# Optimization experiments

Hardware: AMD Instinct MI355X
Metric: run time of the kernel (lower is better)

Reference implementation:

```python
import jax, jax.numpy as jnp
import numpy as np

EPS = 1e-5
elu = jax.nn.elu

def bn(x, g, b):
    # BatchNorm (training-mode stats), channel axis = 1
    axes = tuple(i for i in range(x.ndim) if i != 1)
    m = x.mean(axes, keepdims=True)
    v = x.var(axes, keepdims=True)
    shp = [1] * x.ndim; shp[1] = -1
    return g.reshape(shp) * (x - m) * jax.lax.rsqrt(v + EPS) + b.reshape(shp)

def setup_inputs() -> dict:
    key = jax.random.key(0)
    B, N, M, K, C, H, O = 8, 8192, 2048, 16, 128, 64, 256
    ks = jax.random.split(key, 16)
    d = {}
    d['q_points'] = jax.random.normal(ks[0], (B, 3, M), jnp.float32)
    d['s_points'] = jax.random.normal(ks[1], (B, 3, N), jnp.float32)
    d['s_feats'] = jax.random.normal(ks[2], (B, C, N), jnp.float32)
    d['f1_w'] = jax.random.normal(ks[3], (H, 3), jnp.float32) * 0.1
    d['f1_b'] = jnp.zeros((H,), jnp.float32); d['f1_g'] = jnp.ones((H,), jnp.float32); d['f1_be'] = jnp.zeros((H,), jnp.float32)
    d['f2_w'] = jax.random.normal(ks[4], (H, H), jnp.float32) * 0.1
    d['f2_b'] = jnp.zeros((H,), jnp.float32); d['f2_g'] = jnp.ones((H,), jnp.float32); d['f2_be'] = jnp.zeros((H,), jnp.float32)
    d['stem_w'] = jax.random.normal(ks[5], (K * K, 3, K), jnp.float32) * 0.1
    d['stem_b'] = jnp.zeros((K * K,), jnp.float32); d['stem_g'] = jnp.ones((K * K,), jnp.float32); d['stem_be'] = jnp.zeros((K * K,), jnp.float32)
    d['x1_w'] = jax.random.normal(ks[6], (K, K, K), jnp.float32) * 0.1
    d['x1_b'] = jnp.zeros((K * K,), jnp.float32); d['x1_g'] = jnp.ones((K * K,), jnp.float32); d['x1_be'] = jnp.zeros((K * K,), jnp.float32)
    d['x2_w'] = jax.random.normal(ks[7], (K, K, K), jnp.float32) * 0.1
    d['x2_b'] = jnp.zeros((K * K,), jnp.float32); d['x2_g'] = jnp.ones((K * K,), jnp.float32); d['x2_be'] = jnp.zeros((K * K,), jnp.float32)
    d['dw_w'] = jax.random.normal(ks[8], (C + H, K), jnp.float32) * 0.1
    d['pw_w'] = jax.random.normal(ks[9], (O, C + H), jnp.float32) * 0.1
    d['pw_b'] = jnp.zeros((O,), jnp.float32); d['sep_g'] = jnp.ones((O,), jnp.float32); d['sep_be'] = jnp.zeros((O,), jnp.float32)
    d['neighbor_indices'] = jax.random.randint(ks[10], (B, M, K), 0, N, jnp.int64)
    return d

def reference(q_points, s_points, s_feats, f1_w, f1_b, f1_g, f1_be,
              f2_w, f2_b, f2_g, f2_be, stem_w, stem_b, stem_g, stem_be,
              x1_w, x1_b, x1_g, x1_be, x2_w, x2_b, x2_g, x2_be,
              dw_w, pw_w, pw_b, sep_g, sep_be, neighbor_indices):
    B, _, M = q_points.shape
    K = neighbor_indices.shape[2]
    bidx = jnp.arange(B)[:, None, None]
    # group_gather: [B,3,M,K] neighbor coords, centered on queries
    sp = jnp.swapaxes(s_points, 1, 2)                      # [B,N,3]
    aligned = jnp.transpose(sp[bidx, neighbor_indices], (0, 3, 1, 2)) - q_points[:, :, :, None]
    sf = jnp.swapaxes(s_feats, 1, 2)                       # [B,N,C]
    nbr = jnp.transpose(sf[bidx, neighbor_indices], (0, 3, 1, 2))  # [B,C,M,K]
    # f_shared_mlp: two 1x1 conv blocks (conv -> ELU -> BN)
    h = bn(elu(jnp.einsum('bcmk,oc->bomk', aligned, f1_w) + f1_b[None, :, None, None]), f1_g, f1_be)
    h = bn(elu(jnp.einsum('bcmk,oc->bomk', h, f2_w) + f2_b[None, :, None, None]), f2_g, f2_be)
    nf = jnp.concatenate([nbr, h], axis=1)                 # [B,C+H,M,K]
    # X-transform shared MLP: stem Conv2d(3 -> K*K, (1,K))
    t = jnp.einsum('bcmk,ock->bom', aligned, stem_w) + stem_b[None, :, None]
    t = bn(elu(t), stem_g, stem_be).reshape(B, K, K, M)    # [B,g,j,M]
    for w, bb, g, be in ((x1_w, x1_b, x1_g, x1_be), (x2_w, x2_b, x2_g, x2_be)):
        # grouped Conv2d(K -> K*K, (K,1), groups=K)
        y = jnp.einsum('bgjm,gpj->bgpm', t, w) + bb.reshape(1, K, K, 1)
        y = bn(elu(y.reshape(B, K * K, M)), g, be).reshape(B, K, K, M)
        t = jnp.swapaxes(y, 1, 2)                          # XReshape transpose(1,2)
    x = jnp.transpose(t, (0, 3, 2, 1))                     # [B,M,K,K]
    # batched matmul: feats^T @ X
    qf = jnp.einsum('bcmk,bmkl->bcml', nf, x)              # [B,C+H,M,K]
    # SeparableConv2d (1,K): depthwise over K then pointwise 1x1, ELU, BN
    dw = jnp.einsum('bcmk,ck->bcm', qf, dw_w)
    out = jnp.einsum('bcm,oc->bom', dw, pw_w) + pw_b[None, :, None]
    out = bn(elu(out), sep_g, sep_be)                      # [B,O,M]
    return out
```

## Files before the change

### kernel.cpp

```cpp
#include <hip/hip_runtime.h>
#include <hip/hip_bf16.h>
#include <cstddef>
#include <cstdint>

constexpr int cB = 8, cN = 8192, cM = 2048, cK = 16, cC = 128, cH = 64, cO = 256, cCH = 192;
constexpr int NPTS = cB * cM;
constexpr float cEPS = 1e-5f;

typedef __attribute__((ext_vector_type(8))) short short8;
typedef __attribute__((ext_vector_type(4))) float f32x4;

constexpr size_t ACC_BN1 = 0, ACC_BN2 = 128, ACC_STEM = 256, ACC_X1 = 768, ACC_X2 = 1280, ACC_FIN = 1792;
constexpr size_t OFF_SFT = 8192;
constexpr size_t OFF_H2  = OFF_SFT + (size_t)cB * cN * 64;
constexpr size_t OFF_TST = OFF_H2 + (size_t)NPTS * 512;
constexpr size_t OFF_Y1  = OFF_TST + (size_t)NPTS * 128;
constexpr size_t OFF_Y2  = OFF_Y1 + (size_t)NPTS * 256;
constexpr size_t OFF_AL  = OFF_Y2 + (size_t)NPTS * 128;
constexpr size_t OFF_DW  = OFF_Y1;
constexpr size_t WS_FLOATS = OFF_Y2 + (size_t)NPTS * 256;

__device__ __forceinline__ float eluf(float x) { return x > 0.f ? x : __expf(x) - 1.f; }

__device__ __forceinline__ uint32_t pk2bf(float a, float b) {
    uint32_t ua = __float_as_uint(a); ua += 0x7FFFu + ((ua >> 16) & 1u);
    uint32_t ub = __float_as_uint(b); ub += 0x7FFFu + ((ub >> 16) & 1u);
    return (ua >> 16) | (ub & 0xFFFF0000u);
}
__device__ __forceinline__ float bf_lo(uint32_t u) { return __uint_as_float(u << 16); }
__device__ __forceinline__ float bf_hi(uint32_t u) { return __uint_as_float(u & 0xFFFF0000u); }
__device__ __forceinline__ uint16_t f2bf_u(float a) {
    uint32_t ua = __float_as_uint(a); ua += 0x7FFFu + ((ua >> 16) & 1u);
    return (uint16_t)(ua >> 16);
}

#define WAVE_SYNC() do { asm volatile("s_waitcnt lgkmcnt(0)" ::: "memory"); \
                         __builtin_amdgcn_sched_barrier(0); } while (0)

__global__ __launch_bounds__(256) void k_tr(const float* __restrict__ sf, float* __restrict__ ws) {
    __shared__ float tA[32][33];
    __shared__ float tBt[32][33];
    int b = blockIdx.z, n0 = blockIdx.x * 32, c0 = blockIdx.y * 32;
    int tx = threadIdx.x, ty = threadIdx.y;
    #pragma unroll
    for (int j = 0; j < 32; j += 8) {
        tA[ty + j][tx]  = sf[((size_t)b * cC + (c0 + ty + j)) * cN + n0 + tx];
        tBt[ty + j][tx] = sf[((size_t)b * cC + 64 + (c0 + ty + j)) * cN + n0 + tx];
    }
    __syncthreads();
    uint32_t* out = (uint32_t*)(ws + OFF_SFT);
    #pragma unroll
    for (int j = 0; j < 32; j += 8)
        out[((size_t)b * cN + (n0 + ty + j)) * 64 + c0 + tx] = pk2bf(tA[tx][ty + j], tBt[tx][ty + j]);
}

__global__ __launch_bounds__(256) void kA(const float* __restrict__ qp, const float* __restrict__ sp,
        const float* __restrict__ f1w, const float* __restrict__ f1b,
        const float* __restrict__ stw, const float* __restrict__ stb,
        const int* __restrict__ nidx, float* __restrict__ ws) {
    __shared__ float alw[4][4][48];
    __shared__ __align__(16) uint16_t albs[16][64];
    __shared__ __align__(16) uint16_t tstt[16][256];
    __shared__ float red[640];
    int t = threadIdx.x, lane = t & 63, w = t >> 6;
    int ncol = lane & 15, g = lane >> 4;
    for (int l = t; l < 640; l += 256) red[l] = 0.f;
    __syncthreads();
    short8 bfr[4][2];
    float sbias[4];
    #pragma unroll
    for (int tt = 0; tt < 4; tt++) {
        int o = w*64 + tt*16 + ncol;
        sbias[tt] = stb[o];
        #pragma unroll
        for (int s = 0; s < 2; s++) {
            short8 bb;
            #pragma unroll
            for (int j = 0; j < 8; j++) {
                int Kk = s*32 + g*8 + j;
                bb[j] = (Kk < 48) ? (short)f2bf_u(stw[(size_t)o*48 + Kk]) : (short)0;
            }
            bfr[tt][s] = bb;
        }
    }
    float w0 = f1w[lane*3], w1 = f1w[lane*3+1], w2 = f1w[lane*3+2], fb = f1b[lane];
    int pt0 = blockIdx.x * 16;
    {
        int p = lane >> 4, k = lane & 15;
        int row = w*4 + p;
        int pt = pt0 + row, b = pt >> 11, m = pt & (cM - 1);
        int id = nidx[(size_t)pt * cK + k];
        #pragma unroll
        for (int c = 0; c < 3; c++) {
            float v = sp[((size_t)b*3 + c)*cN + id] - qp[((size_t)b*3 + c)*cM + m];
            alw[w][p][c*16 + k] = v;
            int bo = ((c*16 + k)*2) ^ ((row & 7) << 4);
            *(uint16_t*)((char*)&albs[row][0] + bo) = f2bf_u(v);
        }
        int bo = ((48 + k)*2) ^ ((row & 7) << 4);
        *(uint16_t*)((char*)&albs[row][0] + bo) = 0;
    }
    WAVE_SYNC();
    {
        float* alg = ws + OFF_AL;
        const float* srcA = &alw[w][0][0];
        int ptw = pt0 + w*4;
        #pragma unroll
        for (int i = 0; i < 3; i++)
            alg[(size_t)ptw*48 + i*64 + lane] = srcA[i*64 + lane];
    }
    float ps1 = 0, pss1 = 0;
    #pragma unroll
    for (int p = 0; p < 4; p++) {
        #pragma unroll
        for (int k = 0; k < 16; k++) {
            float a0 = alw[w][p][k], a1 = alw[w][p][16 + k], a2 = alw[w][p][32 + k];
            float e = eluf(fb + w0*a0 + w1*a1 + w2*a2);
            ps1 += e; pss1 += e*e;
        }
    }
    atomicAdd(&red[512 + lane], ps1); atomicAdd(&red[576 + lane], pss1);
    __syncthreads();
    short8 a0, a1;
    {
        int b0 = (g*16) ^ ((ncol & 7) << 4);
        int b1 = (64 + g*16) ^ ((ncol & 7) << 4);
        a0 = *(const short8*)((const char*)&albs[ncol][0] + b0);
        a1 = *(const short8*)((const char*)&albs[ncol][0] + b1);
    }
    #pragma unroll
    for (int tt = 0; tt < 4; tt++) {
        f32x4 acc = {0.f, 0.f, 0.f, 0.f};
        acc = __builtin_amdgcn_mfma_f32_16x16x32_bf16(a0, bfr[tt][0], acc, 0, 0, 0);
        acc = __builtin_amdgcn_mfma_f32_16x16x32_bf16(a1, bfr[tt][1], acc, 0, 0, 0);
        int o = w*64 + tt*16 + ncol;
        float ps2 = 0, pss2 = 0;
        #pragma unroll
        for (int r = 0; r < 4; r++) {
            float e = eluf(acc[r] + sbias[tt]);
            ps2 += e; pss2 += e*e;
            tstt[g*4 + r][o] = f2bf_u(e);
        }
        atomicAdd(&red[o], ps2); atomicAdd(&red[256 + o], pss2);
    }
    __syncthreads();
    {
        uint4* tst4 = (uint4*)(ws + OFF_TST);
        const uint4* srcT = (const uint4*)&tstt[0][0];
        tst4[(size_t)pt0*32 + t]       = srcT[t];
        tst4[(size_t)pt0*32 + 256 + t] = srcT[256 + t];
    }
    atomicAdd(&ws[ACC_STEM + t], red[t]);
    atomicAdd(&ws[ACC_STEM + 256 + t], red[256 + t]);
    if (t < 64) { atomicAdd(&ws[ACC_BN1 + t], red[512 + t]); atomicAdd(&ws[ACC_BN1 + 64 + t], red[576 + t]); }
}

__global__ __launch_bounds__(256) void kC(const float* __restrict__ f1w, const float* __restrict__ f1b,
        const float* __restrict__ f2w, const float* __restrict__ f2b,
        const float* __restrict__ f1g, const float* __restrict__ f1be, float* __restrict__ ws) {
    __shared__ float alw[4][4][48];
    __shared__ __align__(16) unsigned char h1l[4][4][2048];
    __shared__ float s1s[64], sh1s[64], b2s[64];
    __shared__ float red[128];
    int t = threadIdx.x, lane = t & 63, w = t >> 6;
    if (t < 128) red[t] = 0.f;
    if (t < 64) {
        float mn = ws[ACC_BN1 + t] * (1.f/262144.f);
        float vr = ws[ACC_BN1 + 64 + t] * (1.f/262144.f) - mn*mn;
        float s = f1g[t] * rsqrtf(vr + cEPS);
        s1s[t] = s; sh1s[t] = f1be[t] - mn*s;
    }
    __syncthreads();
    float w0 = f1w[lane*3], w1 = f1w[lane*3+1], w2 = f1w[lane*3+2], fb = f1b[lane];
    int ncol = lane & 15, g = lane >> 4;
    if (t < 64) {
        float a = f2b[t];
        const float* fr = f2w + (size_t)t*64;
        #pragma unroll 8
        for (int c = 0; c < 64; c++) a += fr[c] * sh1s[c];
        b2s[t] = a;
    }
    short8 bfr[4][2];
    #pragma unroll
    for (int tt = 0; tt < 4; tt++) {
        int o = tt*16 + ncol;
        #pragma unroll
        for (int s = 0; s < 2; s++) {
            short8 bb;
            #pragma unroll
            for (int j = 0; j < 8; j++) {
                int c = s*32 + g*8 + j;
                bb[j] = (short)f2bf_u(f2w[(size_t)o*64 + c] * s1s[c]);
            }
            bfr[tt][s] = bb;
        }
    }
    __syncthreads();
    float bias2[4];
    #pragma unroll
    for (int tt = 0; tt < 4; tt++) bias2[tt] = b2s[tt*16 + ncol];
    int ptw = blockIdx.x * 16 + w * 4;
    {
        const float* alg = ws + OFF_AL;
        float* dst = &alw[w][0][0];
        #pragma unroll
        for (int i = 0; i < 3; i++)
            dst[i*64 + lane] = alg[(size_t)ptw*48 + i*64 + lane];
    }
    WAVE_SYNC();
    #pragma unroll
    for (int p = 0; p < 4; p++) {
        #pragma unroll
        for (int k = 0; k < 16; k++) {
            float a0 = alw[w][p][k], a1 = alw[w][p][16 + k], a2 = alw[w][p][32 + k];
            float e = eluf(fb + w0*a0 + w1*a1 + w2*a2);
            int byteoff = (lane*2) ^ ((k & 7) << 4);
            *(uint16_t*)&h1l[w][p][k*128 + byteoff] = (uint16_t)f2bf_u(e);
        }
    }
    WAVE_SYNC();
    float ps[4] = {0,0,0,0}, pss[4] = {0,0,0,0};
    int b0o = (g*16) ^ ((ncol & 7) << 4);
    int b1o = (64 + g*16) ^ ((ncol & 7) << 4);
    short8 a0v[4], a1v[4];
    #pragma unroll
    for (int p = 0; p < 4; p++) {
        a0v[p] = *(const short8*)&h1l[w][p][ncol*128 + b0o];
        a1v[p] = *(const short8*)&h1l[w][p][ncol*128 + b1o];
    }
    WAVE_SYNC();
    #pragma unroll
    for (int p = 0; p < 4; p++) {
        #pragma unroll
        for (int tt = 0; tt < 4; tt++) {
            f32x4 acc = {0.f, 0.f, 0.f, 0.f};
            acc = __builtin_amdgcn_mfma_f32_16x16x32_bf16(a0v[p], bfr[tt][0], acc, 0, 0, 0);
            acc = __builtin_amdgcn_mfma_f32_16x16x32_bf16(a1v[p], bfr[tt][1], acc, 0, 0, 0);
            float e0 = eluf(acc[0] + bias2[tt]);
            float e1 = eluf(acc[1] + bias2[tt]);
            float e2 = eluf(acc[2] + bias2[tt]);
            float e3 = eluf(acc[3] + bias2[tt]);
            ps[tt]  += e0+e1+e2+e3;
            pss[tt] += e0*e0+e1*e1+e2*e2+e3*e3;
            int o = tt*16 + ncol;
            *(uint2*)&h1l[w][p][o*32 + g*8] = make_uint2(pk2bf(e0, e1), pk2bf(e2, e3));
        }
    }
    WAVE_SYNC();
    {
        uint4* dst = (uint4*)((uint32_t*)(ws + OFF_H2) + (size_t)ptw*512);
        const uint4* srcH = (const uint4*)&h1l[w][0][0];
        #pragma unroll
        for (int i = 0; i < 8; i++)
            dst[i*64 + lane] = srcH[i*64 + lane];
    }
    #pragma unroll
    for (int tt = 0; tt < 4; tt++) {
        int o = tt*16 + ncol;
        atomicAdd(&red[o], ps[tt]); atomicAdd(&red[64 + o], pss[tt]);
    }
    __syncthreads();
    if (t < 64) { atomicAdd(&ws[ACC_BN2 + t], red[t]); atomicAdd(&ws[ACC_BN2 + 64 + t], red[64 + t]); }
}

__global__ __launch_bounds__(256) void kE(const float* __restrict__ x1w, const float* __restrict__ x1b,
        const float* __restrict__ stg, const float* __restrict__ stbe, float* __restrict__ ws) {
    __shared__ float xw[256 * 17];
    __shared__ float ts[4][4][256];
    __shared__ float red[512];
    int t = threadIdx.x, lane = t & 63, w = t >> 6;
    for (int l = t; l < 4096; l += 256) xw[(l >> 4)*17 + (l & 15)] = x1w[l];
    for (int l = t; l < 512; l += 256) red[l] = 0.f;
    float sscl[4], sshf[4];
    #pragma unroll
    for (int i = 0; i < 4; i++) {
        int ch = lane*4 + i;
        float mn = ws[ACC_STEM + ch] * (1.f/16384.f);
        float vr = ws[ACC_STEM + 256 + ch] * (1.f/16384.f) - mn*mn;
        float s = stg[ch] * rsqrtf(vr + cEPS);
        sscl[i] = s; sshf[i] = stbe[ch] - mn*s;
    }
    __syncthreads();
    const uint16_t* tstb = (const uint16_t*)(ws + OFF_TST);
    int pt0 = blockIdx.x * 16 + w * 4;
    #pragma unroll
    for (int p = 0; p < 4; p++) {
        uint2 v2 = *(const uint2*)&tstb[(size_t)(pt0 + p)*256 + lane*4];
        ts[w][p][lane*4+0] = sscl[0]*bf_lo(v2.x) + sshf[0];
        ts[w][p][lane*4+1] = sscl[1]*bf_hi(v2.x) + sshf[1];
        ts[w][p][lane*4+2] = sscl[2]*bf_lo(v2.y) + sshf[2];
        ts[w][p][lane*4+3] = sscl[3]*bf_hi(v2.y) + sshf[3];
    }
    WAVE_SYNC();
    float eo[4][4];
    #pragma unroll
    for (int sl = 0; sl < 4; sl++) {
        int o = (sl < 2) ? (lane*2 + sl) : (128 + lane*2 + sl - 2);
        int gg = o >> 4;
        float bia = x1b[o];
        float a0 = bia, a1 = bia, a2 = bia, a3 = bia;
        #pragma unroll
        for (int j4 = 0; j4 < 4; j4++) {
            float s0 = xw[o*17 + j4*4], s1 = xw[o*17 + j4*4+1], s2 = xw[o*17 + j4*4+2], s3 = xw[o*17 + j4*4+3];
            float4 t0 = *(const float4*)&ts[w][0][gg*16 + j4*4];
            float4 t1 = *(const float4*)&ts[w][1][gg*16 + j4*4];
            float4 t2 = *(const float4*)&ts[w][2][gg*16 + j4*4];
            float4 t3 = *(const float4*)&ts[w][3][gg*16 + j4*4];
            a0 += s0*t0.x + s1*t0.y + s2*t0.z + s3*t0.w;
            a1 += s0*t1.x + s1*t1.y + s2*t1.z + s3*t1.w;
            a2 += s0*t2.x + s1*t2.y + s2*t2.z + s3*t2.w;
            a3 += s0*t3.x + s1*t3.y + s2*t3.z + s3*t3.w;
        }
        eo[0][sl] = eluf(a0); eo[1][sl] = eluf(a1); eo[2][sl] = eluf(a2); eo[3][sl] = eluf(a3);
        float ps = eo[0][sl]+eo[1][sl]+eo[2][sl]+eo[3][sl];
        float qs = eo[0][sl]*eo[0][sl]+eo[1][sl]*eo[1][sl]+eo[2][sl]*eo[2][sl]+eo[3][sl]*eo[3][sl];
        atomicAdd(&red[o], ps); atomicAdd(&red[256 + o], qs);
    }
    uint32_t* y1p = (uint32_t*)(ws + OFF_Y1);
    #pragma unroll
    for (int p = 0; p < 4; p++) {
        y1p[(size_t)(pt0 + p)*128 + lane]      = pk2bf(eo[p][0], eo[p][1]);
        y1p[(size_t)(pt0 + p)*128 + 64 + lane] = pk2bf(eo[p][2], eo[p][3]);
    }
    __syncthreads();
    atomicAdd(&ws[ACC_X1 + t], red[t]); atomicAdd(&ws[ACC_X1 + 256 + t], red[256 + t]);
}

__global__ __launch_bounds__(256) void kG(const float* __restrict__ x2w, const float* __restrict__ x2b,
        const float* __restrict__ x1g, const float* __restrict__ x1be, float* __restrict__ ws) {
    __shared__ float xw[256 * 17];
    __shared__ float ts[4][4][256];
    __shared__ float red[512];
    int t = threadIdx.x, lane = t & 63, w = t >> 6;
    for (int l = t; l < 4096; l += 256) xw[(l >> 4)*17 + (l & 15)] = x2w[l];
    for (int l = t; l < 512; l += 256) red[l] = 0.f;
    float sscl[4], sshf[4];
    #pragma unroll
    for (int i = 0; i < 4; i++) {
        int ch = lane*4 + i;
        float mn = ws[ACC_X1 + ch] * (1.f/16384.f);
        float vr = ws[ACC_X1 + 256 + ch] * (1.f/16384.f) - mn*mn;
        float s = x1g[ch] * rsqrtf(vr + cEPS);
        sscl[i] = s; sshf[i] = x1be[ch] - mn*s;
    }
    __syncthreads();
    const uint32_t* y1p = (const uint32_t*)(ws + OFF_Y1);
    int pt0 = blockIdx.x * 16 + w * 4;
    #pragma unroll
    for (int p = 0; p < 4; p++) {
        uint2 v2 = *(const uint2*)(y1p + (size_t)(pt0 + p)*128 + lane*2);
        float vv[4] = { sscl[0]*bf_lo(v2.x) + sshf[0], sscl[1]*bf_hi(v2.x) + sshf[1],
                        sscl[2]*bf_lo(v2.y) + sshf[2], sscl[3]*bf_hi(v2.y) + sshf[3] };
        #pragma unroll
        for (int i = 0; i < 4; i++) {
            int ch = lane*4 + i;
            ts[w][p][((ch & 15) << 4) | (ch >> 4)] = vv[i];
        }
    }
    WAVE_SYNC();
    float eo[4][4];
    #pragma unroll
    for (int sl = 0; sl < 4; sl++) {
        int o = (sl < 2) ? (lane*2 + sl) : (128 + lane*2 + sl - 2);
        int gg = o >> 4;
        float bia = x2b[o];
        float a0 = bia, a1 = bia, a2 = bia, a3 = bia;
        #pragma unroll
        for (int j4 = 0; j4 < 4; j4++) {
            float s0 = xw[o*17 + j4*4], s1 = xw[o*17 + j4*4+1], s2 = xw[o*17 + j4*4+2], s3 = xw[o*17 + j4*4+3];
            float4 t0 = *(const float4*)&ts[w][0][gg*16 + j4*4];
            float4 t1 = *(const float4*)&ts[w][1][gg*16 + j4*4];
            float4 t2 = *(const float4*)&ts[w][2][gg*16 + j4*4];
            float4 t3 = *(const float4*)&ts[w][3][gg*16 + j4*4];
            a0 += s0*t0.x + s1*t0.y + s2*t0.z + s3*t0.w;
            a1 += s0*t1.x + s1*t1.y + s2*t1.z + s3*t1.w;
            a2 += s0*t2.x + s1*t2.y + s2*t2.z + s3*t2.w;
            a3 += s0*t3.x + s1*t3.y + s2*t3.z + s3*t3.w;
        }
        eo[0][sl] = eluf(a0); eo[1][sl] = eluf(a1); eo[2][sl] = eluf(a2); eo[3][sl] = eluf(a3);
        float ps = eo[0][sl]+eo[1][sl]+eo[2][sl]+eo[3][sl];
        float qs = eo[0][sl]*eo[0][sl]+eo[1][sl]*eo[1][sl]+eo[2][sl]*eo[2][sl]+eo[3][sl]*eo[3][sl];
        atomicAdd(&red[o], ps); atomicAdd(&red[256 + o], qs);
    }
    uint32_t* y2p = (uint32_t*)(ws + OFF_Y2);
    #pragma unroll
    for (int p = 0; p < 4; p++) {
        y2p[(size_t)(pt0 + p)*128 + lane]      = pk2bf(eo[p][0], eo[p][1]);
        y2p[(size_t)(pt0 + p)*128 + 64 + lane] = pk2bf(eo[p][2], eo[p][3]);
    }
    __syncthreads();
    atomicAdd(&ws[ACC_X2 + t], red[t]); atomicAdd(&ws[ACC_X2 + 256 + t], red[256 + t]);
}

__global__ __launch_bounds__(256) void kI(const float* __restrict__ dww,
        const float* __restrict__ f2g, const float* __restrict__ f2be,
        const float* __restrict__ x2g, const float* __restrict__ x2be,
        const int* __restrict__ nidx, float* __restrict__ ws) {
    __shared__ float dws[192 * 17];
    __shared__ float xs[4][256];
    const uint32_t* h2p = (const uint32_t*)(ws + OFF_H2);
    const uint32_t* sfp = (const uint32_t*)(ws + OFF_SFT);
    const uint32_t* y2p = (const uint32_t*)(ws + OFF_Y2);
    int t = threadIdx.x, lane = t & 63, w = t >> 6;
    for (int l = t; l < 3072; l += 256) dws[(l >> 4)*17 + (l & 15)] = dww[l];
    float sx[4], shx[4];
    #pragma unroll
    for (int i = 0; i < 4; i++) {
        int ch = lane*4 + i;
        float mn = ws[ACC_X2 + ch] * (1.f/16384.f);
        float vr = ws[ACC_X2 + 256 + ch] * (1.f/16384.f) - mn*mn;
        float s = x2g[ch] * rsqrtf(vr + cEPS);
        sx[i] = s; shx[i] = x2be[ch] - mn*s;
    }
    float s2, sh2;
    {
        float mn = ws[ACC_BN2 + lane] * (1.f/262144.f);
        float vr = ws[ACC_BN2 + 64 + lane] * (1.f/262144.f) - mn*mn;
        s2 = f2g[lane] * rsqrtf(vr + cEPS);
        sh2 = f2be[lane] - mn*s2;
    }
    __syncthreads();
    uint16_t* dwb = (uint16_t*)(ws + OFF_DW);
    int pt0 = blockIdx.x * 8 + w * 2;
    for (int p = 0; p < 2; p++) {
        int pt = pt0 + p, b = pt >> 11;
        const int4* ip = (const int4*)(nidx + (size_t)pt * cK);
        int4 iA = ip[0], iB = ip[1], iC2 = ip[2], iD = ip[3];
        int idxv[16] = {iA.x, iA.y, iA.z, iA.w, iB.x, iB.y, iB.z, iB.w,
                        iC2.x, iC2.y, iC2.z, iC2.w, iD.x, iD.y, iD.z, iD.w};
        float nfa[16], nfb[16];
        #pragma unroll
        for (int k = 0; k < 16; k++) {
            uint32_t u = sfp[((size_t)b*cN + idxv[k]) * 64 + lane];
            nfa[k] = bf_lo(u); nfb[k] = bf_hi(u);
        }
        float nfh[16];
        {
            const uint4* srcq = (const uint4*)(h2p + (size_t)pt*512 + lane*8);
            uint4 ha = srcq[0], hbq = srcq[1];
            nfh[0]  = s2*bf_lo(ha.x)  + sh2; nfh[1]  = s2*bf_hi(ha.x)  + sh2;
            nfh[2]  = s2*bf_lo(ha.y)  + sh2; nfh[3]  = s2*bf_hi(ha.y)  + sh2;
            nfh[4]  = s2*bf_lo(ha.z)  + sh2; nfh[5]  = s2*bf_hi(ha.z)  + sh2;
            nfh[6]  = s2*bf_lo(ha.w)  + sh2; nfh[7]  = s2*bf_hi(ha.w)  + sh2;
            nfh[8]  = s2*bf_lo(hbq.x) + sh2; nfh[9]  = s2*bf_hi(hbq.x) + sh2;
            nfh[10] = s2*bf_lo(hbq.y) + sh2; nfh[11] = s2*bf_hi(hbq.y) + sh2;
            nfh[12] = s2*bf_lo(hbq.z) + sh2; nfh[13] = s2*bf_hi(hbq.z) + sh2;
            nfh[14] = s2*bf_lo(hbq.w) + sh2; nfh[15] = s2*bf_hi(hbq.w) + sh2;
        }
        {
            uint2 v2 = *(const uint2*)(y2p + (size_t)pt*128 + lane*2);
            xs[w][lane*4+0] = sx[0]*bf_lo(v2.x) + shx[0];
            xs[w][lane*4+1] = sx[1]*bf_hi(v2.x) + shx[1];
            xs[w][lane*4+2] = sx[2]*bf_lo(v2.y) + shx[2];
            xs[w][lane*4+3] = sx[3]*bf_hi(v2.y) + shx[3];
        }
        WAVE_SYNC();
        float qc[16];
        #pragma unroll
        for (int l = 0; l < 16; l++) qc[l] = 0.f;
        #pragma unroll
        for (int k = 0; k < 16; k++) {
            float4 x0 = *(const float4*)&xs[w][k*16 + 0];
            float4 x1 = *(const float4*)&xs[w][k*16 + 4];
            float4 x2v = *(const float4*)&xs[w][k*16 + 8];
            float4 x3 = *(const float4*)&xs[w][k*16 + 12];
            float nh = nfh[k];
            qc[0] += nh*x0.x; qc[1] += nh*x0.y; qc[2]  += nh*x0.z; qc[3]  += nh*x0.w;
            qc[4] += nh*x1.x; qc[5] += nh*x1.y; qc[6]  += nh*x1.z; qc[7]  += nh*x1.w;
            qc[8] += nh*x2v.x; qc[9] += nh*x2v.y; qc[10] += nh*x2v.z; qc[11] += nh*x2v.w;
            qc[12] += nh*x3.x; qc[13] += nh*x3.y; qc[14] += nh*x3.z; qc[15] += nh*x3.w;
        }
        float dc = 0;
        #pragma unroll
        for (int l = 0; l < 16; l++) dc += qc[l] * dws[(lane + 128)*17 + l];
        float qa[16], qb[16];
        #pragma unroll
        for (int l = 0; l < 16; l++) { qa[l] = 0.f; qb[l] = 0.f; }
        #pragma unroll
        for (int k = 0; k < 16; k++) {
            float4 x0 = *(const float4*)&xs[w][k*16 + 0];
            float4 x1 = *(const float4*)&xs[w][k*16 + 4];
            float4 x2v = *(const float4*)&xs[w][k*16 + 8];
            float4 x3 = *(const float4*)&xs[w][k*16 + 12];
            float na = nfa[k], nb = nfb[k];
            qa[0] += na*x0.x; qa[1] += na*x0.y; qa[2]  += na*x0.z; qa[3]  += na*x0.w;
            qa[4] += na*x1.x; qa[5] += na*x1.y; qa[6]  += na*x1.z; qa[7]  += na*x1.w;
            qa[8] += na*x2v.x; qa[9] += na*x2v.y; qa[10] += na*x2v.z; qa[11] += na*x2v.w;
            qa[12] += na*x3.x; qa[13] += na*x3.y; qa[14] += na*x3.z; qa[15] += na*x3.w;
            qb[0] += nb*x0.x; qb[1] += nb*x0.y; qb[2]  += nb*x0.z; qb[3]  += nb*x0.w;
            qb[4] += nb*x1.x; qb[5] += nb*x1.y; qb[6]  += nb*x1.z; qb[7]  += nb*x1.w;
            qb[8] += nb*x2v.x; qb[9] += nb*x2v.y; qb[10] += nb*x2v.z; qb[11] += nb*x2v.w;
            qb[12] += nb*x3.x; qb[13] += nb*x3.y; qb[14] += nb*x3.z; qb[15] += nb*x3.w;
        }
        float da = 0, db = 0;
        #pragma unroll
        for (int l = 0; l < 16; l++) {
            da += qa[l] * dws[lane*17 + l];
            db += qb[l] * dws[(lane + 64)*17 + l];
        }
        uint16_t* op = dwb + (size_t)pt * cCH;
        op[lane] = f2bf_u(da); op[lane + 64] = f2bf_u(db); op[lane + 128] = f2bf_u(dc);
        WAVE_SYNC();
    }
}

__global__ __launch_bounds__(256) void kJ(const float* __restrict__ pww, const float* __restrict__ pwb,
                                          float* __restrict__ ws, float* __restrict__ out) {
    __shared__ float red[128];
    int t = threadIdx.x, lane = t & 63, w = t >> 6;
    int ncol = lane & 15, g = lane >> 4;
    if (t < 128) red[t] = 0.f;
    __syncthreads();
    int p0 = blockIdx.x * 64;
    int otile = blockIdx.y * 64 + w * 16;
    short8 afr[6];
    #pragma unroll
    for (int kt = 0; kt < 6; kt++) {
        const float* src = pww + (size_t)(otile + ncol) * cCH + kt*32 + g*8;
        float4 v0 = *(const float4*)src;
        float4 v1 = *(const float4*)(src + 4);
        short8 aa;
        aa[0] = (short)f2bf_u(v0.x); aa[1] = (short)f2bf_u(v0.y);
        aa[2] = (short)f2bf_u(v0.z); aa[3] = (short)f2bf_u(v0.w);
        aa[4] = (short)f2bf_u(v1.x); aa[5] = (short)f2bf_u(v1.y);
        aa[6] = (short)f2bf_u(v1.z); aa[7] = (short)f2bf_u(v1.w);
        afr[kt] = aa;
    }
    float pb[4];
    #pragma unroll
    for (int r = 0; r < 4; r++) pb[r] = pwb[otile + g*4 + r];
    const uint16_t* dwb = (const uint16_t*)(ws + OFF_DW);
    int bb = p0 >> 11, mb0 = p0 & (cM - 1);
    float psum[4] = {0,0,0,0}, pssq[4] = {0,0,0,0};
    #pragma unroll
    for (int mt = 0; mt < 4; mt++) {
        const uint16_t* brow = dwb + (size_t)(p0 + mt*16 + ncol) * cCH;
        f32x4 acc = {0.f, 0.f, 0.f, 0.f};
        #pragma unroll
        for (int kt = 0; kt < 6; kt++) {
            short8 bfr = *(const short8*)&brow[kt*32 + g*8];
            acc = __builtin_amdgcn_mfma_f32_16x16x32_bf16(afr[kt], bfr, acc, 0, 0, 0);
        }
        #pragma unroll
        for (int r = 0; r < 4; r++) {
            float e = eluf(acc[r] + pb[r]);
            psum[r] += e; pssq[r] += e*e;
            out[((size_t)bb*cO + otile + g*4 + r)*cM + mb0 + mt*16 + ncol] = e;
        }
    }
    #pragma unroll
    for (int r = 0; r < 4; r++) {
        float s_ = psum[r], q_ = pssq[r];
        #pragma unroll
        for (int off = 1; off < 16; off <<= 1) { s_ += __shfl_xor(s_, off); q_ += __shfl_xor(q_, off); }
        if (ncol == 0) {
            atomicAdd(&red[w*16 + g*4 + r], s_);
            atomicAdd(&red[64 + w*16 + g*4 + r], q_);
        }
    }
    __syncthreads();
    if (t < 64) {
        atomicAdd(&ws[ACC_FIN + blockIdx.y*64 + t], red[t]);
        atomicAdd(&ws[ACC_FIN + 256 + blockIdx.y*64 + t], red[64 + t]);
    }
}

__global__ __launch_bounds__(256) void kK(float* __restrict__ out, const float* __restrict__ ws,
        const float* __restrict__ sepg, const float* __restrict__ sepbe) {
    int i = blockIdx.x * 256 + threadIdx.x;
    if (i < (cB*cO*cM) / 4) {
        int o = (i >> 9) & 255;
        float mn = ws[ACC_FIN + o] * (1.f/16384.f);
        float vr = ws[ACC_FIN + 256 + o] * (1.f/16384.f) - mn*mn;
        float s = sepg[o] * rsqrtf(vr + cEPS);
        float sh = sepbe[o] - mn*s;
        float4 v = ((float4*)out)[i];
        v.x = s*v.x + sh; v.y = s*v.y + sh; v.z = s*v.z + sh; v.w = s*v.w + sh;
        ((float4*)out)[i] = v;
    }
}

extern "C" void kernel_launch(void* const* d_in, const int* in_sizes, int n_in,
                              void* d_out, int out_size, void* d_ws, size_t ws_size,
                              hipStream_t stream) {
    const float* qp   = (const float*)d_in[0];
    const float* sp   = (const float*)d_in[1];
    const float* sf   = (const float*)d_in[2];
    const float* f1w  = (const float*)d_in[3];
    const float* f1b  = (const float*)d_in[4];
    const float* f1g  = (const float*)d_in[5];
    const float* f1be = (const float*)d_in[6];
    const float* f2w  = (const float*)d_in[7];
    const float* f2b  = (const float*)d_in[8];
    const float* f2g  = (const float*)d_in[9];
    const float* f2be = (const float*)d_in[10];
    const float* stw  = (const float*)d_in[11];
    const float* stb  = (const float*)d_in[12];
    const float* stg  = (const float*)d_in[13];
    const float* stbe = (const float*)d_in[14];
    const float* x1w  = (const float*)d_in[15];
    const float* x1b  = (const float*)d_in[16];
    const float* x1g  = (const float*)d_in[17];
    const float* x1be = (const float*)d_in[18];
    const float* x2w  = (const float*)d_in[19];
    const float* x2b  = (const float*)d_in[20];
    const float* x2g  = (const float*)d_in[21];
    const float* x2be = (const float*)d_in[22];
    const float* dww  = (const float*)d_in[23];
    const float* pww  = (const float*)d_in[24];
    const float* pwb  = (const float*)d_in[25];
    const float* sepg = (const float*)d_in[26];
    const float* sepbe= (const float*)d_in[27];
    const int*   nidx = (const int*)d_in[28];
    float* ws  = (float*)d_ws;
    float* out = (float*)d_out;
    if (ws_size < WS_FLOATS * sizeof(float)) return;

    hipMemsetAsync(d_ws, 0, 2304 * sizeof(float), stream);
    k_tr<<<dim3(cN/32, 2, cB), dim3(32, 8), 0, stream>>>(sf, ws);
    kA<<<NPTS/16, 256, 0, stream>>>(qp, sp, f1w, f1b, stw, stb, nidx, ws);
    kC<<<NPTS/16, 256, 0, stream>>>(f1w, f1b, f2w, f2b, f1g, f1be, ws);
    kE<<<NPTS/16, 256, 0, stream>>>(x1w, x1b, stg, stbe, ws);
    kG<<<NPTS/16, 256, 0, stream>>>(x2w, x2b, x1g, x1be, ws);
    kI<<<NPTS/8,  256, 0, stream>>>(dww, f2g, f2be, x2g, x2be, nidx, ws);
    kJ<<<dim3(NPTS/64, cO/64), 256, 0, stream>>>(pww, pwb, ws, out);
    kK<<<(cB*cO*cM/4 + 255)/256, 256, 0, stream>>>(out, ws, sepg, sepbe);
}
```

Before: 244.6 us.

## Merge independent kernels into block-partitioned launches to overlap transpose and stages

Folds the feature transpose into kA as extra blocks, and runs kC and kE together in one launch, picking the branch from the block index. The stages merged in each pair have no data dependency on each other, so they can run concurrently, filling the GPU better and saving launch gaps. kC also now writes h2 straight to global memory instead of staging it through LDS. The cost is that the merged kernels get the union of shared-memory footprints (about 37 KB for kCE), which can lower occupancy for the lighter branch.

```diff
diff --git a/kernel.cpp b/kernel.cpp
--- a/kernel.cpp
+++ b/kernel.cpp
@@ -37,32 +37,36 @@
 #define WAVE_SYNC() do { asm volatile("s_waitcnt lgkmcnt(0)" ::: "memory"); \
                          __builtin_amdgcn_sched_barrier(0); } while (0)
 
-__global__ __launch_bounds__(256) void k_tr(const float* __restrict__ sf, float* __restrict__ ws) {
-    __shared__ float tA[32][33];
-    __shared__ float tBt[32][33];
-    int b = blockIdx.z, n0 = blockIdx.x * 32, c0 = blockIdx.y * 32;
-    int tx = threadIdx.x, ty = threadIdx.y;
-    #pragma unroll
-    for (int j = 0; j < 32; j += 8) {
-        tA[ty + j][tx]  = sf[((size_t)b * cC + (c0 + ty + j)) * cN + n0 + tx];
-        tBt[ty + j][tx] = sf[((size_t)b * cC + 64 + (c0 + ty + j)) * cN + n0 + tx];
-    }
-    __syncthreads();
-    uint32_t* out = (uint32_t*)(ws + OFF_SFT);
-    #pragma unroll
-    for (int j = 0; j < 32; j += 8)
-        out[((size_t)b * cN + (n0 + ty + j)) * 64 + c0 + tx] = pk2bf(tA[tx][ty + j], tBt[tx][ty + j]);
-}
-
-__global__ __launch_bounds__(256) void kA(const float* __restrict__ qp, const float* __restrict__ sp,
+__global__ __launch_bounds__(256) void kAT(const float* __restrict__ qp, const float* __restrict__ sp,
         const float* __restrict__ f1w, const float* __restrict__ f1b,
         const float* __restrict__ stw, const float* __restrict__ stb,
-        const int* __restrict__ nidx, float* __restrict__ ws) {
-    __shared__ float alw[4][4][48];
-    __shared__ __align__(16) uint16_t albs[16][64];
-    __shared__ __align__(16) uint16_t tstt[16][256];
-    __shared__ float red[640];
-    int t = threadIdx.x, lane = t & 63, w = t >> 6;
+        const float* __restrict__ sf, const int* __restrict__ nidx, float* __restrict__ ws) {
+    __shared__ __align__(16) unsigned char smem[15872];
+    int t = threadIdx.x;
+    if (blockIdx.x >= 1024) {
+        float* tA = (float*)smem;
+        float* tB = (float*)(smem + 4224);
+        int id = blockIdx.x - 1024;
+        int n0 = (id & 255) * 32, c0 = ((id >> 8) & 1) * 32, b = id >> 9;
+        int tx = t & 31, ty = t >> 5;
+        #pragma unroll
+        for (int j = 0; j < 32; j += 8) {
+            tA[(ty + j)*33 + tx] = sf[((size_t)b * cC + (c0 + ty + j)) * cN + n0 + tx];
+            tB[(ty + j)*33 + tx] = sf[((size_t)b * cC + 64 + (c0 + ty + j)) * cN + n0 + tx];
+        }
+        __syncthreads();
+        uint32_t* outp = (uint32_t*)(ws + OFF_SFT);
+        #pragma unroll
+        for (int j = 0; j < 32; j += 8)
+            outp[((size_t)b * cN + (n0 + ty + j)) * 64 + c0 + tx] =
+                pk2bf(tA[tx*33 + ty + j], tB[tx*33 + ty + j]);
+        return;
+    }
+    float (*alw)[4][48]   = (float(*)[4][48])smem;
+    uint16_t (*albs)[64]  = (uint16_t(*)[64])(smem + 3072);
+    uint16_t (*tstt)[256] = (uint16_t(*)[256])(smem + 5120);
+    float* red            = (float*)(smem + 13312);
+    int lane = t & 63, w = t >> 6;
     int ncol = lane & 15, g = lane >> 4;
     for (int l = t; l < 640; l += 256) red[l] = 0.f;
     __syncthreads();
@@ -155,175 +159,175 @@
     if (t < 64) { atomicAdd(&ws[ACC_BN1 + t], red[512 + t]); atomicAdd(&ws[ACC_BN1 + 64 + t], red[576 + t]); }
 }
 
-__global__ __launch_bounds__(256) void kC(const float* __restrict__ f1w, const float* __restrict__ f1b,
+__global__ __launch_bounds__(256) void kCE(const float* __restrict__ f1w, const float* __restrict__ f1b,
         const float* __restrict__ f2w, const float* __restrict__ f2b,
-        const float* __restrict__ f1g, const float* __restrict__ f1be, float* __restrict__ ws) {
-    __shared__ float alw[4][4][48];
-    __shared__ __align__(16) unsigned char h1l[4][4][2048];
-    __shared__ float s1s[64], sh1s[64], b2s[64];
-    __shared__ float red[128];
+        const float* __restrict__ f1g, const float* __restrict__ f1be,
+        const float* __restrict__ x1w, const float* __restrict__ x1b,
+        const float* __restrict__ stg, const float* __restrict__ stbe, float* __restrict__ ws) {
+    __shared__ __align__(16) unsigned char smem[37120];
     int t = threadIdx.x, lane = t & 63, w = t >> 6;
-    if (t < 128) red[t] = 0.f;
-    if (t < 64) {
-        float mn = ws[ACC_BN1 + t] * (1.f/262144.f);
-        float vr = ws[ACC_BN1 + 64 + t] * (1.f/262144.f) - mn*mn;
-        float s = f1g[t] * rsqrtf(vr + cEPS);
-        s1s[t] = s; sh1s[t] = f1be[t] - mn*s;
-    }
-    __syncthreads();
-    float w0 = f1w[lane*3], w1 = f1w[lane*3+1], w2 = f1w[lane*3+2], fb = f1b[lane];
-    int ncol = lane & 15, g = lane >> 4;
-    if (t < 64) {
-        float a = f2b[t];
-        const float* fr = f2w + (size_t)t*64;
-        #pragma unroll 8
-        for (int c = 0; c < 64; c++) a += fr[c] * sh1s[c];
-        b2s[t] = a;
-    }
-    short8 bfr[4][2];
-    #pragma unroll
-    for (int tt = 0; tt < 4; tt++) {
-        int o = tt*16 + ncol;
-        #pragma unroll
-        for (int s = 0; s < 2; s++) {
-            short8 bb;
+    if (blockIdx.x < 1024) {
+        float (*alw)[4][48] = (float(*)[4][48])smem;
+        unsigned char (*h1l)[4][2048] = (unsigned char(*)[4][2048])(smem + 3072);
+        float* s1s  = (float*)(smem + 35840);
+        float* sh1s = (float*)(smem + 36096);
+        float* b2s  = (float*)(smem + 36352);
+        float* red  = (float*)(smem + 36608);
+        if (t < 128) red[t] = 0.f;
+        if (t < 64) {
+            float mn = ws[ACC_BN1 + t] * (1.f/262144.f);
+            float vr = ws[ACC_BN1 + 64 + t] * (1.f/262144.f) - mn*mn;
+            float s = f1g[t] * rsqrtf(vr + cEPS);
+            s1s[t] = s; sh1s[t] = f1be[t] - mn*s;
+        }
+        __syncthreads();
+        float w0 = f1w[lane*3], w1 = f1w[lane*3+1], w2 = f1w[lane*3+2], fb = f1b[lane];
+        int ncol = lane & 15, g = lane >> 4;
+        if (t < 64) {
+            float a = f2b[t];
+            const float* fr = f2w + (size_t)t*64;
+            #pragma unroll 8
+            for (int c = 0; c < 64; c++) a += fr[c] * sh1s[c];
+            b2s[t] = a;
+        }
+        short8 bfr[4][2];
+        #pragma unroll
+        for (int tt = 0; tt < 4; tt++) {
+            int o = tt*16 + ncol;
             #pragma unroll
-            for (int j = 0; j < 8; j++) {
-                int c = s*32 + g*8 + j;
-                bb[j] = (short)f2bf_u(f2w[(size_t)o*64 + c] * s1s[c]);
+            for (int s = 0; s < 2; s++) {
+                short8 bb;
+                #pragma unroll
+                for (int j = 0; j < 8; j++) {
+                    int c = s*32 + g*8 + j;
+                    bb[j] = (short)f2bf_u(f2w[(size_t)o*64 + c] * s1s[c]);
+                }
+                bfr[tt][s] = bb;
             }
-            bfr[tt][s] = bb;
-        }
-    }
-    __syncthreads();
-    float bias2[4];
-    #pragma unroll
-    for (int tt = 0; tt < 4; tt++) bias2[tt] = b2s[tt*16 + ncol];
-    int ptw = blockIdx.x * 16 + w * 4;
+        }
+        __syncthreads();
+        float bias2[4];
+        #pragma unroll
+        for (int tt = 0; tt < 4; tt++) bias2[tt] = b2s[tt*16 + ncol];
+        int ptw = blockIdx.x * 16 + w * 4;
+        {
+            const float* alg = ws + OFF_AL;
+            float* dst = &alw[w][0][0];
+            #pragma unroll
+            for (int i = 0; i < 3; i++)
+                dst[i*64 + lane] = alg[(size_t)ptw*48 + i*64 + lane];
+        }
+        WAVE_SYNC();
+        #pragma unroll
+        for (int p = 0; p < 4; p++) {
+            #pragma unroll
+            for (int k = 0; k < 16; k++) {
+                float a0 = alw[w][p][k], a1 = alw[w][p][16 + k], a2 = alw[w][p][32 + k];
+                float e = eluf(fb + w0*a0 + w1*a1 + w2*a2);
+                int byteoff = (lane*2) ^ ((k & 7) << 4);
+                *(uint16_t*)&h1l[w][p][k*128 + byteoff] = (uint16_t)f2bf_u(e);
+            }
+        }
+        WAVE_SYNC();
+        float ps[4] = {0,0,0,0}, pss[4] = {0,0,0,0};
+        int b0o = (g*16) ^ ((ncol & 7) << 4);
+        int b1o = (64 + g*16) ^ ((ncol & 7) << 4);
+        short8 a0v[4], a1v[4];
+        #pragma unroll
+        for (int p = 0; p < 4; p++) {
+            a0v[p] = *(const short8*)&h1l[w][p][ncol*128 + b0o];
+            a1v[p] = *(const short8*)&h1l[w][p][ncol*128 + b1o];
+        }
+        WAVE_SYNC();
+        uint32_t* h2p = (uint32_t*)(ws + OFF_H2);
+        #pragma unroll
+        for (int p = 0; p < 4; p++) {
+            int pt = ptw + p;
+            #pragma unroll
+            for (int tt = 0; tt < 4; tt++) {
+                f32x4 acc = {0.f, 0.f, 0.f, 0.f};
+                acc = __builtin_amdgcn_mfma_f32_16x16x32_bf16(a0v[p], bfr[tt][0], acc, 0, 0, 0);
+                acc = __builtin_amdgcn_mfma_f32_16x16x32_bf16(a1v[p], bfr[tt][1], acc, 0, 0, 0);
+                float e0 = eluf(acc[0] + bias2[tt]);
+                float e1 = eluf(acc[1] + bias2[tt]);
+                float e2 = eluf(acc[2] + bias2[tt]);
+                float e3 = eluf(acc[3] + bias2[tt]);
+                ps[tt]  += e0+e1+e2+e3;
+                pss[tt] += e0*e0+e1*e1+e2*e2+e3*e3;
+                int o = tt*16 + ncol;
+                *(uint2*)(h2p + (size_t)pt*512 + o*8 + g*2) = make_uint2(pk2bf(e0, e1), pk2bf(e2, e3));
+            }
+        }
+        #pragma unroll
+        for (int tt = 0; tt < 4; tt++) {
+            int o = tt*16 + ncol;
+            atomicAdd(&red[o], ps[tt]); atomicAdd(&red[64 + o], pss[tt]);
+        }
+        __syncthreads();
+        if (t < 64) { atomicAdd(&ws[ACC_BN2 + t], red[t]); atomicAdd(&ws[ACC_BN2 + 64 + t], red[64 + t]); }
+        return;
+    }
     {
-        const float* alg = ws + OFF_AL;
-        float* dst = &alw[w][0][0];
-        #pragma unroll
-        for (int i = 0; i < 3; i++)
-            dst[i*64 + lane] = alg[(size_t)ptw*48 + i*64 + lane];
-    }
-    WAVE_SYNC();
-    #pragma unroll
-    for (int p = 0; p < 4; p++) {
-        #pragma unroll
-        for (int k = 0; k < 16; k++) {
-            float a0 = alw[w][p][k], a1 = alw[w][p][16 + k], a2 = alw[w][p][32 + k];
-            float e = eluf(fb + w0*a0 + w1*a1 + w2*a2);
-            int byteoff = (lane*2) ^ ((k & 7) << 4);
-            *(uint16_t*)&h1l[w][p][k*128 + byteoff] = (uint16_t)f2bf_u(e);
-        }
-    }
-    WAVE_SYNC();
-    float ps[4] = {0,0,0,0}, pss[4] = {0,0,0,0};
-    int b0o = (g*16) ^ ((ncol & 7) << 4);
-    int b1o = (64 + g*16) ^ ((ncol & 7) << 4);
-    short8 a0v[4], a1v[4];
-    #pragma unroll
-    for (int p = 0; p < 4; p++) {
-        a0v[p] = *(const short8*)&h1l[w][p][ncol*128 + b0o];
-        a1v[p] = *(const short8*)&h1l[w][p][ncol*128 + b1o];
-    }
-    WAVE_SYNC();
-    #pragma unroll
-    for (int p = 0; p < 4; p++) {
-        #pragma unroll
-        for (int tt = 0; tt < 4; tt++) {
-            f32x4 acc = {0.f, 0.f, 0.f, 0.f};
-            acc = __builtin_amdgcn_mfma_f32_16x16x32_bf16(a0v[p], bfr[tt][0], acc, 0, 0, 0);
-            acc = __builtin_amdgcn_mfma_f32_16x16x32_bf16(a1v[p], bfr[tt][1], acc, 0, 0, 0);
-            float e0 = eluf(acc[0] + bias2[tt]);
-            float e1 = eluf(acc[1] + bias2[tt]);
-            float e2 = eluf(acc[2] + bias2[tt]);
-            float e3 = eluf(acc[3] + bias2[tt]);
-            ps[tt]  += e0+e1+e2+e3;
-            pss[tt] += e0*e0+e1*e1+e2*e2+e3*e3;
-            int o = tt*16 + ncol;
-            *(uint2*)&h1l[w][p][o*32 + g*8] = make_uint2(pk2bf(e0, e1), pk2bf(e2, e3));
-        }
-    }
-    WAVE_SYNC();
-    {
-        uint4* dst = (uint4*)((uint32_t*)(ws + OFF_H2) + (size_t)ptw*512);
-        const uint4* srcH = (const uint4*)&h1l[w][0][0];
-        #pragma unroll
-        for (int i = 0; i < 8; i++)
-            dst[i*64 + lane] = srcH[i*64 + lane];
-    }
-    #pragma unroll
-    for (int tt = 0; tt < 4; tt++) {
-        int o = tt*16 + ncol;
-        atomicAdd(&red[o], ps[tt]); atomicAdd(&red[64 + o], pss[tt]);
-    }
-    __syncthreads();
-    if (t < 64) { atomicAdd(&ws[ACC_BN2 + t], red[t]); atomicAdd(&ws[ACC_BN2 + 64 + t], red[64 + t]); }
-}
-
-__global__ __launch_bounds__(256) void kE(const float* __restrict__ x1w, const float* __restrict__ x1b,
-        const float* __restrict__ stg, const float* __restrict__ stbe, float* __restrict__ ws) {
-    __shared__ float xw[256 * 17];
-    __shared__ float ts[4][4][256];
-    __shared__ float red[512];
-    int t = threadIdx.x, lane = t & 63, w = t >> 6;
-    for (int l = t; l < 4096; l += 256) xw[(l >> 4)*17 + (l & 15)] = x1w[l];
-    for (int l = t; l < 512; l += 256) red[l] = 0.f;
-    float sscl[4], sshf[4];
-    #pragma unroll
-    for (int i = 0; i < 4; i++) {
-        int ch = lane*4 + i;
-        float mn = ws[ACC_STEM + ch] * (1.f/16384.f);
-        float vr = ws[ACC_STEM + 256 + ch] * (1.f/16384.f) - mn*mn;
-        float s = stg[ch] * rsqrtf(vr + cEPS);
-        sscl[i] = s; sshf[i] = stbe[ch] - mn*s;
-    }
-    __syncthreads();
-    const uint16_t* tstb = (const uint16_t*)(ws + OFF_TST);
-    int pt0 = blockIdx.x * 16 + w * 4;
-    #pragma unroll
-    for (int p = 0; p < 4; p++) {
-        uint2 v2 = *(const uint2*)&tstb[(size_t)(pt0 + p)*256 + lane*4];
-        ts[w][p][lane*4+0] = sscl[0]*bf_lo(v2.x) + sshf[0];
-        ts[w][p][lane*4+1] = sscl[1]*bf_hi(v2.x) + sshf[1];
-        ts[w][p][lane*4+2] = sscl[2]*bf_lo(v2.y) + sshf[2];
-        ts[w][p][lane*4+3] = sscl[3]*bf_hi(v2.y) + sshf[3];
-    }
-    WAVE_SYNC();
-    float eo[4][4];
-    #pragma unroll
-    for (int sl = 0; sl < 4; sl++) {
-        int o = (sl < 2) ? (lane*2 + sl) : (128 + lane*2 + sl - 2);
-        int gg = o >> 4;
-        float bia = x1b[o];
-        float a0 = bia, a1 = bia, a2 = bia, a3 = bia;
-        #pragma unroll
-        for (int j4 = 0; j4 < 4; j4++) {
-            float s0 = xw[o*17 + j4*4], s1 = xw[o*17 + j4*4+1], s2 = xw[o*17 + j4*4+2], s3 = xw[o*17 + j4*4+3];
-            float4 t0 = *(const float4*)&ts[w][0][gg*16 + j4*4];
-            float4 t1 = *(const float4*)&ts[w][1][gg*16 + j4*4];
-            float4 t2 = *(const float4*)&ts[w][2][gg*16 + j4*4];
-            float4 t3 = *(const float4*)&ts[w][3][gg*16 + j4*4];
-            a0 += s0*t0.x + s1*t0.y + s2*t0.z + s3*t0.w;
-            a1 += s0*t1.x + s1*t1.y + s2*t1.z + s3*t1.w;
-            a2 += s0*t2.x + s1*t2.y + s2*t2.z + s3*t2.w;
-            a3 += s0*t3.x + s1*t3.y + s2*t3.z + s3*t3.w;
-        }
-        eo[0][sl] = eluf(a0); eo[1][sl] = eluf(a1); eo[2][sl] = eluf(a2); eo[3][sl] = eluf(a3);
-        float ps = eo[0][sl]+eo[1][sl]+eo[2][sl]+eo[3][sl];
-        float qs = eo[0][sl]*eo[0][sl]+eo[1][sl]*eo[1][sl]+eo[2][sl]*eo[2][sl]+eo[3][sl]*eo[3][sl];
-        atomicAdd(&red[o], ps); atomicAdd(&red[256 + o], qs);
-    }
-    uint32_t* y1p = (uint32_t*)(ws + OFF_Y1);
-    #pragma unroll
-    for (int p = 0; p < 4; p++) {
-        y1p[(size_t)(pt0 + p)*128 + lane]      = pk2bf(eo[p][0], eo[p][1]);
-        y1p[(size_t)(pt0 + p)*128 + 64 + lane] = pk2bf(eo[p][2], eo[p][3]);
-    }
-    __syncthreads();
-    atomicAdd(&ws[ACC_X1 + t], red[t]); atomicAdd(&ws[ACC_X1 + 256 + t], red[256 + t]);
+        float* xw = (float*)smem;
+        float (*ts)[4][256] = (float(*)[4][256])(smem + 17408);
+        float* red = (float*)(smem + 33792);
+        int bid = blockIdx.x - 1024;
+        for (int l = t; l < 4096; l += 256) xw[(l >> 4)*17 + (l & 15)] = x1w[l];
+        for (int l = t; l < 512; l += 256) red[l] = 0.f;
+        float sscl[4], sshf[4];
+        #pragma unroll
+        for (int i = 0; i < 4; i++) {
+            int ch = lane*4 + i;
+            float mn = ws[ACC_STEM + ch] * (1.f/16384.f);
+            float vr = ws[ACC_STEM + 256 + ch] * (1.f/16384.f) - mn*mn;
+            float s = stg[ch] * rsqrtf(vr + cEPS);
+            sscl[i] = s; sshf[i] = stbe[ch] - mn*s;
+        }
+        __syncthreads();
+        const uint16_t* tstb = (const uint16_t*)(ws + OFF_TST);
+        int pt0 = bid * 16 + w * 4;
+        #pragma unroll
+        for (int p = 0; p < 4; p++) {
+            uint2 v2 = *(const uint2*)&tstb[(size_t)(pt0 + p)*256 + lane*4];
+            ts[w][p][lane*4+0] = sscl[0]*bf_lo(v2.x) + sshf[0];
+            ts[w][p][lane*4+1] = sscl[1]*bf_hi(v2.x) + sshf[1];
+            ts[w][p][lane*4+2] = sscl[2]*bf_lo(v2.y) + sshf[2];
+            ts[w][p][lane*4+3] = sscl[3]*bf_hi(v2.y) + sshf[3];
+        }
+        WAVE_SYNC();
+        float eo[4][4];
+        #pragma unroll
+        for (int sl = 0; sl < 4; sl++) {
+            int o = (sl < 2) ? (lane*2 + sl) : (128 + lane*2 + sl - 2);
+            int gg = o >> 4;
+            float bia = x1b[o];
+            float a0 = bia, a1 = bia, a2 = bia, a3 = bia;
+            #pragma unroll
+            for (int j4 = 0; j4 < 4; j4++) {
+                float s0 = xw[o*17 + j4*4], s1 = xw[o*17 + j4*4+1], s2 = xw[o*17 + j4*4+2], s3 = xw[o*17 + j4*4+3];
+                float4 t0 = *(const float4*)&ts[w][0][gg*16 + j4*4];
+                float4 t1 = *(const float4*)&ts[w][1][gg*16 + j4*4];
+                float4 t2 = *(const float4*)&ts[w][2][gg*16 + j4*4];
+                float4 t3 = *(const float4*)&ts[w][3][gg*16 + j4*4];
+                a0 += s0*t0.x + s1*t0.y + s2*t0.z + s3*t0.w;
+                a1 += s0*t1.x + s1*t1.y + s2*t1.z + s3*t1.w;
+                a2 += s0*t2.x + s1*t2.y + s2*t2.z + s3*t2.w;
+                a3 += s0*t3.x + s1*t3.y + s2*t3.z + s3*t3.w;
+            }
+            eo[0][sl] = eluf(a0); eo[1][sl] = eluf(a1); eo[2][sl] = eluf(a2); eo[3][sl] = eluf(a3);
+            float ps = eo[0][sl]+eo[1][sl]+eo[2][sl]+eo[3][sl];
+            float qs = eo[0][sl]*eo[0][sl]+eo[1][sl]*eo[1][sl]+eo[2][sl]*eo[2][sl]+eo[3][sl]*eo[3][sl];
+            atomicAdd(&red[o], ps); atomicAdd(&red[256 + o], qs);
+        }
+        uint32_t* y1p = (uint32_t*)(ws + OFF_Y1);
+        #pragma unroll
+        for (int p = 0; p < 4; p++) {
+            y1p[(size_t)(pt0 + p)*128 + lane]      = pk2bf(eo[p][0], eo[p][1]);
+            y1p[(size_t)(pt0 + p)*128 + 64 + lane] = pk2bf(eo[p][2], eo[p][3]);
+        }
+        __syncthreads();
+        atomicAdd(&ws[ACC_X1 + t], red[t]); atomicAdd(&ws[ACC_X1 + 256 + t], red[256 + t]);
+    }
 }
 
 __global__ __launch_bounds__(256) void kG(const float* __restrict__ x2w, const float* __restrict__ x2b,
@@ -617,10 +621,8 @@
     if (ws_size < WS_FLOATS * sizeof(float)) return;
 
     hipMemsetAsync(d_ws, 0, 2304 * sizeof(float), stream);
-    k_tr<<<dim3(cN/32, 2, cB), dim3(32, 8), 0, stream>>>(sf, ws);
-    kA<<<NPTS/16, 256, 0, stream>>>(qp, sp, f1w, f1b, stw, stb, nidx, ws);
-    kC<<<NPTS/16, 256, 0, stream>>>(f1w, f1b, f2w, f2b, f1g, f1be, ws);
-    kE<<<NPTS/16, 256, 0, stream>>>(x1w, x1b, stg, stbe, ws);
+    kAT<<<1024 + 4096, 256, 0, stream>>>(qp, sp, f1w, f1b, stw, stb, sf, nidx, ws);
+    kCE<<<2048, 256, 0, stream>>>(f1w, f1b, f2w, f2b, f1g, f1be, x1w, x1b, stg, stbe, ws);
     kG<<<NPTS/16, 256, 0, stream>>>(x2w, x2b, x1g, x1be, ws);
     kI<<<NPTS/8,  256, 0, stream>>>(dww, f2g, f2be, x2g, x2be, nidx, ws);
     kJ<<<dim3(NPTS/64, cO/64), 256, 0, stream>>>(pww, pwb, ws, out);
```

After: 230.5 us. 1.06x faster.
